# Kernel tuning notes

Hardware: AMD Instinct MI355X
Metric: run time of the kernel (lower is better)

Reference implementation:

```python
import jax, jax.numpy as jnp
import numpy as np


def _max_pairwise_dist(l, r):
    # l: [N, d], r: [M, d]
    # squared distances via Gram trick: ||l||^2 + ||r||^2 - 2 l.r  -> [N, M]
    l_sq = jnp.sum(l * l, axis=-1)  # [N]
    r_sq = jnp.sum(r * r, axis=-1)  # [M]
    cross = jnp.einsum('nd,md->nm', l, r)  # [N, M]
    sq_dists = l_sq[:, None] + r_sq[None, :] - 2.0 * cross
    sq_dists = jnp.maximum(sq_dists, 0.0)  # guard tiny negatives
    return jnp.sqrt(jnp.max(sq_dists))  # sqrt of max == max of sqrt (monotone)


def setup_inputs() -> dict:
    key = jax.random.key(0)
    k1, k2 = jax.random.split(key)
    N, M, D = 8192, 8192, 64
    return {
        'l_dfa_embeddings': jax.random.normal(k1, (N, D), dtype=jnp.float32),
        'r_dfa_embeddings': jax.random.normal(k2, (M, D), dtype=jnp.float32),
    }


def reference(l_dfa_embeddings, r_dfa_embeddings):
    # Max over all pairwise L2 distances between l and r state embeddings
    return _max_pairwise_dist(l_dfa_embeddings, r_dfa_embeddings)
```

## Files before the change

kernel.cpp:

```cpp
#include <hip/hip_runtime.h>
#include <hip/hip_bf16.h>
#include <math.h>


typedef __attribute__((ext_vector_type(8)))  short  short8;
typedef __attribute__((ext_vector_type(4)))  float  f32x4;
typedef __attribute__((ext_vector_type(16))) float  f32x16;

constexpr int D  = 64;
constexpr int NR = 8192;
constexpr int NBLK = 16 * 32;

__device__ __forceinline__ short f2bf(float f) {
    __hip_bfloat16 h = __float2bfloat16(f);
    return __builtin_bit_cast(short, h);
}


__global__ __launch_bounds__(256) void prepack_kernel(
    const float* __restrict__ L, const float* __restrict__ R,
    short* __restrict__ Apk, short* __restrict__ Bpk,
    float* __restrict__ lsq, float* __restrict__ rsq)
{
    const int t = blockIdx.x * 256 + threadIdx.x;
    const int r = t >> 3;
    const int j = t & 7;
    const int kk = j >> 1, kh = j & 1;
    const bool isL = (r < NR);
    const int rr = isL ? r : r - NR;

    const float* src = (isL ? L : R) + (size_t)rr * D + j * 8;
    short* pk = isL ? Apk : Bpk;

    f32x4 v0 = *reinterpret_cast<const f32x4*>(src + 0);
    f32x4 v1 = *reinterpret_cast<const f32x4*>(src + 4);

    float p = 0.f;
    #pragma unroll
    for (int e = 0; e < 4; ++e) { p = fmaf(v0[e], v0[e], p); p = fmaf(v1[e], v1[e], p); }

    short8 w;
    #pragma unroll
    for (int e = 0; e < 4; ++e) { w[e] = f2bf(v0[e]); w[4+e] = f2bf(v1[e]); }
    *reinterpret_cast<short8*>(
        pk + ((size_t)(rr >> 5) * 4 + kk) * 512 + (kh * 32 + (rr & 31)) * 8) = w;

    p += __shfl_xor(p, 1, 64);
    p += __shfl_xor(p, 2, 64);
    p += __shfl_xor(p, 4, 64);
    if (j == 0) (isL ? lsq : rsq)[rr] = p;
}

__global__ __launch_bounds__(256, 2) void pairdist_mfma_kernel(
    const short* __restrict__ Apk, const short* __restrict__ Bpk,
    const float* __restrict__ lsq, const float* __restrict__ rsq,
    float* __restrict__ slots)
{
    __shared__ __align__(16) short A_lds[2][4][4][64][8];
    __shared__ __align__(16) short B_lds[4][4][64][8];
    __shared__ __align__(16) float lsq_s[512];
    __shared__ __align__(16) float rsq_s[256];
    __shared__ float wmax_s[4];

    const int tid  = threadIdx.x;
    const int lane = tid & 63;
    const int wave = tid >> 6;
    const int xc = blockIdx.x;
    const int yb = blockIdx.y;

    const size_t Abase = (size_t)(xc * 16) * 2048;

    {
        const short* At = Apk + Abase;
        #pragma unroll
        for (int i = 0; i < 4; ++i)
            __builtin_amdgcn_global_load_lds(
                (const __attribute__((address_space(1))) unsigned int*)
                    (At + ((size_t)i * 4 + wave) * 512 + lane * 8),
                (__attribute__((address_space(3))) unsigned int*)
                    (&A_lds[0][i][wave][0][0]),
                16, 0, 0);
    }
    {
        #pragma unroll
        for (int s = 0; s < 4; ++s) {
            const int gsrc = yb * 8 + (s >> 1) * 4 + 2 + (s & 1);
            __builtin_amdgcn_global_load_lds(
                (const __attribute__((address_space(1))) unsigned int*)
                    (Bpk + ((size_t)gsrc * 4 + wave) * 512 + lane * 8),
                (__attribute__((address_space(3))) unsigned int*)
                    (&B_lds[s][wave][0][0]),
                16, 0, 0);
        }
    }

    lsq_s[tid]       = lsq[xc * 512 + tid];
    lsq_s[256 + tid] = lsq[xc * 512 + 256 + tid];
    rsq_s[tid]       = rsq[yb * 256 + tid];

    const int wm = wave >> 1;
    const int wn = wave & 1;
    short8 bf[2][4];
    #pragma unroll
    for (int nj = 0; nj < 2; ++nj)
        #pragma unroll
        for (int kk = 0; kk < 4; ++kk)
            bf[nj][kk] = *reinterpret_cast<const short8*>(
                Bpk + ((size_t)(yb * 8 + wn * 4 + nj) * 4 + kk) * 512 + lane * 8);

    __syncthreads();

    const int col = lane & 31;
    const int h   = lane >> 5;
    float rq[4];
    #pragma unroll
    for (int nj = 0; nj < 4; ++nj) rq[nj] = rsq_s[wn * 128 + nj * 32 + col];

    float lmax = 0.f;
    int cur = 0;
    for (int t = 0; t < 4; ++t) {
        if (t < 3) {
            const short* At = Apk + Abase + (size_t)(t + 1) * 8192;
            #pragma unroll
            for (int i = 0; i < 4; ++i)
                __builtin_amdgcn_global_load_lds(
                    (const __attribute__((address_space(1))) unsigned int*)
                        (At + ((size_t)i * 4 + wave) * 512 + lane * 8),
                    (__attribute__((address_space(3))) unsigned int*)
                        (&A_lds[cur ^ 1][i][wave][0][0]),
                    16, 0, 0);
            __builtin_amdgcn_sched_barrier(0);
        }

        f32x16 acc[2][4] = {};
        #pragma unroll
        for (int kk = 0; kk < 4; ++kk) {
            short8 a0 = *reinterpret_cast<const short8*>(&A_lds[cur][wm*2+0][kk][lane][0]);
            short8 a1 = *reinterpret_cast<const short8*>(&A_lds[cur][wm*2+1][kk][lane][0]);
            short8 b2 = *reinterpret_cast<const short8*>(&B_lds[wn*2+0][kk][lane][0]);
            short8 b3 = *reinterpret_cast<const short8*>(&B_lds[wn*2+1][kk][lane][0]);
            acc[0][0] = __builtin_amdgcn_mfma_f32_32x32x16_bf16(a0, bf[0][kk], acc[0][0], 0, 0, 0);
            acc[0][1] = __builtin_amdgcn_mfma_f32_32x32x16_bf16(a0, bf[1][kk], acc[0][1], 0, 0, 0);
            acc[0][2] = __builtin_amdgcn_mfma_f32_32x32x16_bf16(a0, b2,        acc[0][2], 0, 0, 0);
            acc[0][3] = __builtin_amdgcn_mfma_f32_32x32x16_bf16(a0, b3,        acc[0][3], 0, 0, 0);
            acc[1][0] = __builtin_amdgcn_mfma_f32_32x32x16_bf16(a1, bf[0][kk], acc[1][0], 0, 0, 0);
            acc[1][1] = __builtin_amdgcn_mfma_f32_32x32x16_bf16(a1, bf[1][kk], acc[1][1], 0, 0, 0);
            acc[1][2] = __builtin_amdgcn_mfma_f32_32x32x16_bf16(a1, b2,        acc[1][2], 0, 0, 0);
            acc[1][3] = __builtin_amdgcn_mfma_f32_32x32x16_bf16(a1, b3,        acc[1][3], 0, 0, 0);
        }

        #pragma unroll
        for (int mi = 0; mi < 2; ++mi) {
            const int rbase = t * 128 + (wm * 2 + mi) * 32 + 4 * h;
            f32x4 lq[4];
            lq[0] = *reinterpret_cast<const f32x4*>(&lsq_s[rbase +  0]);
            lq[1] = *reinterpret_cast<const f32x4*>(&lsq_s[rbase +  8]);
            lq[2] = *reinterpret_cast<const f32x4*>(&lsq_s[rbase + 16]);
            lq[3] = *reinterpret_cast<const f32x4*>(&lsq_s[rbase + 24]);
            #pragma unroll
            for (int nj = 0; nj < 4; ++nj) {
                float x[16];
                #pragma unroll
                for (int g = 0; g < 4; ++g)
                    #pragma unroll
                    for (int e = 0; e < 4; ++e)
                        x[g*4+e] = fmaf(-2.f, acc[mi][nj][g*4+e], lq[g][e]);
                float y0 = fmaxf(x[0],  x[1]),  y1 = fmaxf(x[2],  x[3]);
                float y2 = fmaxf(x[4],  x[5]),  y3 = fmaxf(x[6],  x[7]);
                float y4 = fmaxf(x[8],  x[9]),  y5 = fmaxf(x[10], x[11]);
                float y6 = fmaxf(x[12], x[13]), y7 = fmaxf(x[14], x[15]);
                float z0 = fmaxf(y0, y1), z1 = fmaxf(y2, y3);
                float z2 = fmaxf(y4, y5), z3 = fmaxf(y6, y7);
                float m  = fmaxf(fmaxf(z0, z1), fmaxf(z2, z3));
                lmax = fmaxf(lmax, m + rq[nj]);
            }
        }

        __syncthreads();
        cur ^= 1;
    }

    #pragma unroll
    for (int off = 32; off >= 1; off >>= 1)
        lmax = fmaxf(lmax, __shfl_xor(lmax, off, 64));
    if (lane == 0) wmax_s[wave] = lmax;
    __syncthreads();
    if (tid == 0) {
        float bmax = fmaxf(fmaxf(wmax_s[0], wmax_s[1]), fmaxf(wmax_s[2], wmax_s[3]));
        slots[blockIdx.y * gridDim.x + blockIdx.x] = fmaxf(bmax, 0.f);
    }
}

__global__ __launch_bounds__(512) void finalize_kernel(
    const float* __restrict__ slots, float* __restrict__ out)
{
    __shared__ float wred[8];
    const int tid = threadIdx.x;
    float v = slots[tid];
    #pragma unroll
    for (int off = 32; off >= 1; off >>= 1)
        v = fmaxf(v, __shfl_xor(v, off, 64));
    if ((tid & 63) == 0) wred[tid >> 6] = v;
    __syncthreads();
    if (tid == 0) {
        float m = wred[0];
        #pragma unroll
        for (int i = 1; i < 8; ++i) m = fmaxf(m, wred[i]);
        out[0] = sqrtf(m);
    }
}

extern "C" void kernel_launch(void* const* d_in, const int* in_sizes, int n_in,
                              void* d_out, int out_size, void* d_ws, size_t ws_size,
                              hipStream_t stream) {
    const float* L = (const float*)d_in[0];
    const float* R = (const float*)d_in[1];

    short* Apk = (short*)d_ws;
    short* Bpk = Apk + (size_t)NR * D;
    float* lsqg = (float*)(Bpk + (size_t)NR * D);
    float* rsqg = lsqg + NR;
    float* slots = rsqg + NR;

    prepack_kernel<<<(2 * NR * 8) / 256, 256, 0, stream>>>(L, R, Apk, Bpk, lsqg, rsqg);
    pairdist_mfma_kernel<<<dim3(16, 32), dim3(256), 0, stream>>>(Apk, Bpk, lsqg, rsqg, slots);
    finalize_kernel<<<1, 512, 0, stream>>>(slots, (float*)d_out);
}
```

Baseline: 21.87 us.

## Split row tiles across more blocks and drop the in-block A-tile pipeline

Each block now computes a single 128x256 tile rather than looping over four 128-row A tiles with double-buffered LDS loads. The grid grows from 512 to 2048 blocks, with x and y swapped so the B-column index is the fast dimension, and the finalize kernel reduces four slots per thread. The aim is more parallelism and lower per-block LDS use, which should let more blocks stay resident. In exchange, B tiles and rsq are reloaded four times as often, the in-block overlap of loads with MFMA is gone, and there are more block launches plus a larger final reduction.

```diff
diff --git a/kernel.cpp b/kernel.cpp
--- a/kernel.cpp
+++ b/kernel.cpp
@@ -9,7 +9,9 @@
 
 constexpr int D  = 64;
 constexpr int NR = 8192;
-constexpr int NBLK = 16 * 32;
+constexpr int GX = 32;
+constexpr int GY = 64;
+constexpr int NSLOT = GX * GY;
 
 __device__ __forceinline__ short f2bf(float f) {
     __hip_bfloat16 h = __float2bfloat16(f);
@@ -56,29 +58,27 @@
     const float* __restrict__ lsq, const float* __restrict__ rsq,
     float* __restrict__ slots)
 {
-    __shared__ __align__(16) short A_lds[2][4][4][64][8];
+    __shared__ __align__(16) short A_lds[4][4][64][8];
     __shared__ __align__(16) short B_lds[4][4][64][8];
-    __shared__ __align__(16) float lsq_s[512];
+    __shared__ __align__(16) float lsq_s[128];
     __shared__ __align__(16) float rsq_s[256];
     __shared__ float wmax_s[4];
 
     const int tid  = threadIdx.x;
     const int lane = tid & 63;
     const int wave = tid >> 6;
-    const int xc = blockIdx.x;
-    const int yb = blockIdx.y;
-
-    const size_t Abase = (size_t)(xc * 16) * 2048;
+    const int yb = blockIdx.x;
+    const int xc = blockIdx.y;
 
     {
-        const short* At = Apk + Abase;
+        const short* At = Apk + (size_t)(xc * 4) * 2048;
         #pragma unroll
         for (int i = 0; i < 4; ++i)
             __builtin_amdgcn_global_load_lds(
                 (const __attribute__((address_space(1))) unsigned int*)
                     (At + ((size_t)i * 4 + wave) * 512 + lane * 8),
                 (__attribute__((address_space(3))) unsigned int*)
-                    (&A_lds[0][i][wave][0][0]),
+                    (&A_lds[i][wave][0][0]),
                 16, 0, 0);
     }
     {
@@ -94,9 +94,8 @@
         }
     }
 
-    lsq_s[tid]       = lsq[xc * 512 + tid];
-    lsq_s[256 + tid] = lsq[xc * 512 + 256 + tid];
-    rsq_s[tid]       = rsq[yb * 256 + tid];
+    if (tid < 128) lsq_s[tid] = lsq[xc * 128 + tid];
+    rsq_s[tid] = rsq[yb * 256 + tid];
 
     const int wm = wave >> 1;
     const int wn = wave & 1;
@@ -116,68 +115,49 @@
     #pragma unroll
     for (int nj = 0; nj < 4; ++nj) rq[nj] = rsq_s[wn * 128 + nj * 32 + col];
 
+    f32x16 acc[2][4] = {};
+    #pragma unroll
+    for (int kk = 0; kk < 4; ++kk) {
+        short8 a0 = *reinterpret_cast<const short8*>(&A_lds[wm*2+0][kk][lane][0]);
+        short8 a1 = *reinterpret_cast<const short8*>(&A_lds[wm*2+1][kk][lane][0]);
+        short8 b2 = *reinterpret_cast<const short8*>(&B_lds[wn*2+0][kk][lane][0]);
+        short8 b3 = *reinterpret_cast<const short8*>(&B_lds[wn*2+1][kk][lane][0]);
+        acc[0][0] = __builtin_amdgcn_mfma_f32_32x32x16_bf16(a0, bf[0][kk], acc[0][0], 0, 0, 0);
+        acc[0][1] = __builtin_amdgcn_mfma_f32_32x32x16_bf16(a0, bf[1][kk], acc[0][1], 0, 0, 0);
+        acc[0][2] = __builtin_amdgcn_mfma_f32_32x32x16_bf16(a0, b2,        acc[0][2], 0, 0, 0);
+        acc[0][3] = __builtin_amdgcn_mfma_f32_32x32x16_bf16(a0, b3,        acc[0][3], 0, 0, 0);
+        acc[1][0] = __builtin_amdgcn_mfma_f32_32x32x16_bf16(a1, bf[0][kk], acc[1][0], 0, 0, 0);
+        acc[1][1] = __builtin_amdgcn_mfma_f32_32x32x16_bf16(a1, bf[1][kk], acc[1][1], 0, 0, 0);
+        acc[1][2] = __builtin_amdgcn_mfma_f32_32x32x16_bf16(a1, b2,        acc[1][2], 0, 0, 0);
+        acc[1][3] = __builtin_amdgcn_mfma_f32_32x32x16_bf16(a1, b3,        acc[1][3], 0, 0, 0);
+    }
+
     float lmax = 0.f;
-    int cur = 0;
-    for (int t = 0; t < 4; ++t) {
-        if (t < 3) {
-            const short* At = Apk + Abase + (size_t)(t + 1) * 8192;
+    #pragma unroll
+    for (int mi = 0; mi < 2; ++mi) {
+        const int rbase = (wm * 2 + mi) * 32 + 4 * h;
+        f32x4 lq[4];
+        lq[0] = *reinterpret_cast<const f32x4*>(&lsq_s[rbase +  0]);
+        lq[1] = *reinterpret_cast<const f32x4*>(&lsq_s[rbase +  8]);
+        lq[2] = *reinterpret_cast<const f32x4*>(&lsq_s[rbase + 16]);
+        lq[3] = *reinterpret_cast<const f32x4*>(&lsq_s[rbase + 24]);
+        #pragma unroll
+        for (int nj = 0; nj < 4; ++nj) {
+            float x[16];
             #pragma unroll
-            for (int i = 0; i < 4; ++i)
-                __builtin_amdgcn_global_load_lds(
-                    (const __attribute__((address_space(1))) unsigned int*)
-                        (At + ((size_t)i * 4 + wave) * 512 + lane * 8),
-                    (__attribute__((address_space(3))) unsigned int*)
-                        (&A_lds[cur ^ 1][i][wave][0][0]),
-                    16, 0, 0);
-            __builtin_amdgcn_sched_barrier(0);
+            for (int g = 0; g < 4; ++g)
+                #pragma unroll
+                for (int e = 0; e < 4; ++e)
+                    x[g*4+e] = fmaf(-2.f, acc[mi][nj][g*4+e], lq[g][e]);
+            float y0 = fmaxf(x[0],  x[1]),  y1 = fmaxf(x[2],  x[3]);
+            float y2 = fmaxf(x[4],  x[5]),  y3 = fmaxf(x[6],  x[7]);
+            float y4 = fmaxf(x[8],  x[9]),  y5 = fmaxf(x[10], x[11]);
+            float y6 = fmaxf(x[12], x[13]), y7 = fmaxf(x[14], x[15]);
+            float z0 = fmaxf(y0, y1), z1 = fmaxf(y2, y3);
+            float z2 = fmaxf(y4, y5), z3 = fmaxf(y6, y7);
+            float m  = fmaxf(fmaxf(z0, z1), fmaxf(z2, z3));
+            lmax = fmaxf(lmax, m + rq[nj]);
         }
-
-        f32x16 acc[2][4] = {};
-        #pragma unroll
-        for (int kk = 0; kk < 4; ++kk) {
-            short8 a0 = *reinterpret_cast<const short8*>(&A_lds[cur][wm*2+0][kk][lane][0]);
-            short8 a1 = *reinterpret_cast<const short8*>(&A_lds[cur][wm*2+1][kk][lane][0]);
-            short8 b2 = *reinterpret_cast<const short8*>(&B_lds[wn*2+0][kk][lane][0]);
-            short8 b3 = *reinterpret_cast<const short8*>(&B_lds[wn*2+1][kk][lane][0]);
-            acc[0][0] = __builtin_amdgcn_mfma_f32_32x32x16_bf16(a0, bf[0][kk], acc[0][0], 0, 0, 0);
-            acc[0][1] = __builtin_amdgcn_mfma_f32_32x32x16_bf16(a0, bf[1][kk], acc[0][1], 0, 0, 0);
-            acc[0][2] = __builtin_amdgcn_mfma_f32_32x32x16_bf16(a0, b2,        acc[0][2], 0, 0, 0);
-            acc[0][3] = __builtin_amdgcn_mfma_f32_32x32x16_bf16(a0, b3,        acc[0][3], 0, 0, 0);
-            acc[1][0] = __builtin_amdgcn_mfma_f32_32x32x16_bf16(a1, bf[0][kk], acc[1][0], 0, 0, 0);
-            acc[1][1] = __builtin_amdgcn_mfma_f32_32x32x16_bf16(a1, bf[1][kk], acc[1][1], 0, 0, 0);
-            acc[1][2] = __builtin_amdgcn_mfma_f32_32x32x16_bf16(a1, b2,        acc[1][2], 0, 0, 0);
-            acc[1][3] = __builtin_amdgcn_mfma_f32_32x32x16_bf16(a1, b3,        acc[1][3], 0, 0, 0);
-        }
-
-        #pragma unroll
-        for (int mi = 0; mi < 2; ++mi) {
-            const int rbase = t * 128 + (wm * 2 + mi) * 32 + 4 * h;
-            f32x4 lq[4];
-            lq[0] = *reinterpret_cast<const f32x4*>(&lsq_s[rbase +  0]);
-            lq[1] = *reinterpret_cast<const f32x4*>(&lsq_s[rbase +  8]);
-            lq[2] = *reinterpret_cast<const f32x4*>(&lsq_s[rbase + 16]);
-            lq[3] = *reinterpret_cast<const f32x4*>(&lsq_s[rbase + 24]);
-            #pragma unroll
-            for (int nj = 0; nj < 4; ++nj) {
-                float x[16];
-                #pragma unroll
-                for (int g = 0; g < 4; ++g)
-                    #pragma unroll
-                    for (int e = 0; e < 4; ++e)
-                        x[g*4+e] = fmaf(-2.f, acc[mi][nj][g*4+e], lq[g][e]);
-                float y0 = fmaxf(x[0],  x[1]),  y1 = fmaxf(x[2],  x[3]);
-                float y2 = fmaxf(x[4],  x[5]),  y3 = fmaxf(x[6],  x[7]);
-                float y4 = fmaxf(x[8],  x[9]),  y5 = fmaxf(x[10], x[11]);
-                float y6 = fmaxf(x[12], x[13]), y7 = fmaxf(x[14], x[15]);
-                float z0 = fmaxf(y0, y1), z1 = fmaxf(y2, y3);
-                float z2 = fmaxf(y4, y5), z3 = fmaxf(y6, y7);
-                float m  = fmaxf(fmaxf(z0, z1), fmaxf(z2, z3));
-                lmax = fmaxf(lmax, m + rq[nj]);
-            }
-        }
-
-        __syncthreads();
-        cur ^= 1;
     }
 
     #pragma unroll
@@ -187,7 +167,7 @@
     __syncthreads();
     if (tid == 0) {
         float bmax = fmaxf(fmaxf(wmax_s[0], wmax_s[1]), fmaxf(wmax_s[2], wmax_s[3]));
-        slots[blockIdx.y * gridDim.x + blockIdx.x] = fmaxf(bmax, 0.f);
+        slots[blockIdx.y * GX + blockIdx.x] = fmaxf(bmax, 0.f);
     }
 }
 
@@ -198,6 +178,9 @@
     const int tid = threadIdx.x;
     float v = slots[tid];
     #pragma unroll
+    for (int i = 1; i < NSLOT / 512; ++i)
+        v = fmaxf(v, slots[tid + i * 512]);
+    #pragma unroll
     for (int off = 32; off >= 1; off >>= 1)
         v = fmaxf(v, __shfl_xor(v, off, 64));
     if ((tid & 63) == 0) wred[tid >> 6] = v;
@@ -223,6 +206,6 @@
     float* slots = rsqg + NR;
 
     prepack_kernel<<<(2 * NR * 8) / 256, 256, 0, stream>>>(L, R, Apk, Bpk, lsqg, rsqg);
-    pairdist_mfma_kernel<<<dim3(16, 32), dim3(256), 0, stream>>>(Apk, Bpk, lsqg, rsqg, slots);
+    pairdist_mfma_kernel<<<dim3(GX, GY), dim3(256), 0, stream>>>(Apk, Bpk, lsqg, rsqg, slots);
     finalize_kernel<<<1, 512, 0, stream>>>(slots, (float*)d_out);
 }
```

Measured after the change: 24.08 us. 10.1% more time.
